# Kernel tuning notes

Hardware: AMD Instinct MI355X
Metric: run time of the kernel (lower is better)

## Reference

```python
import jax, jax.numpy as jnp
import numpy as np

N = 50000        # nodes
E = 800000       # edges (avg degree 16)
HID = 96         # hidden_channels
HEADS = 4        # heads passed to SRGATConv
D = HID // HEADS # per-head dim
R = 38           # num_relations
NEG_SLOPE = 0.2  # LeakyReLU slope for attention logits


def setup_inputs() -> dict:
    key = jax.random.key(0)
    ks = jax.random.split(key, 9)
    x = jax.random.normal(ks[0], (N, HID), jnp.float32)
    edge_index = jax.random.randint(ks[1], (2, E), 0, N, dtype=jnp.int32)
    edge_type = jax.random.randint(ks[2], (E,), 0, R, dtype=jnp.int32)
    s = 1.0 / np.sqrt(HID)
    W = jax.random.normal(ks[3], (HID, HID), jnp.float32) * s          # node projection
    rel_emb = jax.random.normal(ks[4], (R, HID), jnp.float32) * s      # relation embeddings
    att_src = jax.random.normal(ks[5], (HEADS, D), jnp.float32) * 0.1  # attention vectors
    att_dst = jax.random.normal(ks[6], (HEADS, D), jnp.float32) * 0.1
    att_rel = jax.random.normal(ks[7], (HEADS, D), jnp.float32) * 0.1
    bias = jnp.zeros((HID,), jnp.float32)
    return {"x": x, "edge_index": edge_index, "edge_type": edge_type,
            "W": W, "rel_emb": rel_emb, "att_src": att_src,
            "att_dst": att_dst, "att_rel": att_rel, "bias": bias}


def reference(x, edge_index, edge_type, W, rel_emb, att_src, att_dst, att_rel, bias):
    # SRGATConv: relation-aware multi-head graph attention, then GELU wrapper.
    n = x.shape[0]
    src, dst = edge_index[0], edge_index[1]
    h = (x @ W).reshape(n, HEADS, D)                    # [N,H,D]
    r = rel_emb[edge_type].reshape(-1, HEADS, D)        # [E,H,D] gathered relation feats
    h_src = h[src]                                      # [E,H,D] irregular gather
    h_dst = h[dst]
    # attention logits per edge/head
    logits = ((h_src * att_src).sum(-1)
              + (h_dst * att_dst).sum(-1)
              + (r * att_rel).sum(-1))                  # [E,H]
    logits = jax.nn.leaky_relu(logits, NEG_SLOPE)
    # segment softmax over incoming edges of each destination node
    lmax = jax.ops.segment_max(logits, dst, num_segments=n)   # [N,H]
    e = jnp.exp(logits - lmax[dst])
    denom = jax.ops.segment_sum(e, dst, num_segments=n)       # [N,H]
    alpha = e / denom[dst]                                    # [E,H]
    # weighted message scatter
    msg = alpha[:, :, None] * (h_src + r)                     # [E,H,D]
    out = jax.ops.segment_sum(msg, dst, num_segments=n).reshape(n, HID) + bias
    out = jax.nn.gelu(out)
    return out, alpha
```

## Files before the change

kernel.cpp:

```cpp
#include <hip/hip_runtime.h>
#include <hip/hip_fp16.h>
#include <math.h>

#define HIDC 96
#define HEADS 4
#define RMAX 40
#define BINSZ 64
#define BINB 6
#define BINCAP 1344
#define TILE 2048
#define SRCB 18
#define SRCM ((1 << SRCB) - 1)
#define ETB 6
#define NBMAX 1024

typedef unsigned u32x2 __attribute__((ext_vector_type(2)));

__device__ __forceinline__ __half2 u2h2(unsigned u) {
    return *reinterpret_cast<__half2*>(&u);
}
__device__ __forceinline__ unsigned h22u(__half2 h) {
    return *reinterpret_cast<unsigned*>(&h);
}

__global__ __launch_bounds__(192) void gemm96(const float* __restrict__ x,
                                              const float* __restrict__ W,
                                              __half* __restrict__ h16,
                                              int* __restrict__ bincnt,
                                              int4* __restrict__ csrtail,
                                              int n, int nbins) {
    for (int i = blockIdx.x * 192 + threadIdx.x; i < nbins; i += gridDim.x * 192)
        bincnt[i] = 0;
    if (blockIdx.x == 0 && threadIdx.x < 16)
        csrtail[threadIdx.x] = make_int4(0, 0, 0, 0);

    __shared__ float Ws[HIDC * HIDC];
    __shared__ float xs[32 * HIDC];
    for (int i = threadIdx.x; i < HIDC * HIDC / 4; i += 192)
        reinterpret_cast<float4*>(Ws)[i] = reinterpret_cast<const float4*>(W)[i];
    int c4 = threadIdx.x % 24;
    int r0 = (threadIdx.x / 24) * 4;
    const float4* xs4 = reinterpret_cast<const float4*>(xs);
    const float4* Ws4 = reinterpret_cast<const float4*>(Ws);
    uint2* h8 = reinterpret_cast<uint2*>(h16);
    int numTiles = (n + 31) >> 5;
    for (int tile = blockIdx.x; tile < numTiles; tile += gridDim.x) {
        int row0 = tile << 5;
        int rows = min(32, n - row0);
        __syncthreads();
        for (int i = threadIdx.x; i < rows * 24; i += 192)
            reinterpret_cast<float4*>(xs)[i] =
                reinterpret_cast<const float4*>(x + (size_t)row0 * HIDC)[i];
        __syncthreads();
        float4 acc[4];
#pragma unroll
        for (int i = 0; i < 4; ++i) acc[i] = make_float4(0.f, 0.f, 0.f, 0.f);
#pragma unroll 4
        for (int k4 = 0; k4 < 24; ++k4) {
            float4 xv[4], wv[4];
#pragma unroll
            for (int i = 0; i < 4; ++i) xv[i] = xs4[(r0 + i) * 24 + k4];
#pragma unroll
            for (int j = 0; j < 4; ++j) wv[j] = Ws4[(k4 * 4 + j) * 24 + c4];
#pragma unroll
            for (int i = 0; i < 4; ++i) {
                const float xi[4] = {xv[i].x, xv[i].y, xv[i].z, xv[i].w};
#pragma unroll
                for (int j = 0; j < 4; ++j) {
                    acc[i].x = fmaf(xi[j], wv[j].x, acc[i].x);
                    acc[i].y = fmaf(xi[j], wv[j].y, acc[i].y);
                    acc[i].z = fmaf(xi[j], wv[j].z, acc[i].z);
                    acc[i].w = fmaf(xi[j], wv[j].w, acc[i].w);
                }
            }
        }
#pragma unroll
        for (int i = 0; i < 4; ++i)
            if (r0 + i < rows) {
                __half2 lo = __floats2half2_rn(acc[i].x, acc[i].y);
                __half2 hi = __floats2half2_rn(acc[i].z, acc[i].w);
                uint2 pk;
                pk.x = h22u(lo);
                pk.y = h22u(hi);
                h8[(size_t)(row0 + r0 + i) * 24 + c4] = pk;
            }
    }
}

__global__ __launch_bounds__(256) void node_dots(
    const __half* __restrict__ h16,
    const float* __restrict__ att_src, const float* __restrict__ att_dst,
    const float* __restrict__ rel, const float* __restrict__ att_rel,
    float4* __restrict__ ps, float* __restrict__ pdi,
    float4* __restrict__ pr, int n, int R_) {
    if (blockIdx.x == gridDim.x - 1) {
        int t = threadIdx.x;
        if (t < R_) {
            const float4* rp = reinterpret_cast<const float4*>(rel + (size_t)t * HIDC);
            const float4* ar = reinterpret_cast<const float4*>(att_rel);
            float acc[HEADS] = {0, 0, 0, 0};
#pragma unroll
            for (int c = 0; c < 24; ++c) {
                float4 v = rp[c], a = ar[c];
                acc[c / 6] += v.x * a.x + v.y * a.y + v.z * a.z + v.w * a.w;
            }
            pr[t] = make_float4(acc[0], acc[1], acc[2], acc[3]);
        }
        return;
    }
    int i = blockIdx.x * blockDim.x + threadIdx.x;
    if (i >= n) return;
    const uint2* hp = reinterpret_cast<const uint2*>(h16 + (size_t)i * HIDC);
    const float4* as = reinterpret_cast<const float4*>(att_src);
    const float4* ad = reinterpret_cast<const float4*>(att_dst);
    float accs[HEADS] = {0, 0, 0, 0}, accd[HEADS] = {0, 0, 0, 0};
#pragma unroll
    for (int c = 0; c < 24; ++c) {
        uint2 hv = hp[c];
        float2 f0 = __half22float2(u2h2(hv.x));
        float2 f1 = __half22float2(u2h2(hv.y));
        float4 a = as[c], d = ad[c];
        int hh = c / 6;
        accs[hh] += f0.x * a.x + f0.y * a.y + f1.x * a.z + f1.y * a.w;
        accd[hh] += f0.x * d.x + f0.y * d.y + f1.x * d.z + f1.y * d.w;
    }
    ps[i] = make_float4(accs[0], accs[1], accs[2], accs[3]);
    *reinterpret_cast<float4*>(pdi + (size_t)i * 8) =
        make_float4(accd[0], accd[1], accd[2], accd[3]);
}

__device__ __forceinline__ float4 ev4(float4 a, float4 b, float4 c) {
    float l0 = a.x + b.x + c.x, l1 = a.y + b.y + c.y;
    float l2 = a.z + b.z + c.z, l3 = a.w + b.w + c.w;
    l0 = l0 >= 0.f ? l0 : 0.2f * l0;
    l1 = l1 >= 0.f ? l1 : 0.2f * l1;
    l2 = l2 >= 0.f ? l2 : 0.2f * l2;
    l3 = l3 >= 0.f ? l3 : 0.2f * l3;
    return make_float4(__expf(l0), __expf(l1), __expf(l2), __expf(l3));
}

__device__ __forceinline__ float gelu_f(float v) {
    float u = 0.7978845608028654f * (v + 0.044715f * v * v * v);
    u = fminf(fmaxf(u, -15.f), 15.f);
    float t = __expf(2.f * u);
    return 0.5f * v * (1.f + (t - 1.f) / (t + 1.f));
}

__global__ __launch_bounds__(256) void bin_edges(
    const int* __restrict__ src, const int* __restrict__ dst,
    const int* __restrict__ et,
    int* __restrict__ bincnt, int* __restrict__ binwords,
    int E_, int nbins) {
    __shared__ int hist[NBMAX];
    __shared__ int base[NBMAX];
    int e0 = blockIdx.x * TILE;
    for (int i = threadIdx.x; i < nbins; i += 256) hist[i] = 0;
    __syncthreads();
    int mybin[8], myrank[8], myword[8];
#pragma unroll
    for (int u = 0; u < 8; ++u) {
        int e = e0 + u * 256 + threadIdx.x;
        mybin[u] = -1;
        if (e < E_) {
            int d = dst[e];
            int b = d >> BINB;
            myword[u] = src[e] | (et[e] << SRCB) | ((d & (BINSZ - 1)) << (SRCB + ETB));
            mybin[u] = b;
            myrank[u] = atomicAdd(&hist[b], 1);
        }
    }
    __syncthreads();
    for (int i = threadIdx.x; i < nbins; i += 256)
        base[i] = hist[i] > 0 ? atomicAdd(&bincnt[i], hist[i]) : 0;
    __syncthreads();
#pragma unroll
    for (int u = 0; u < 8; ++u) {
        if (mybin[u] >= 0) {
            int pos = base[mybin[u]] + myrank[u];
            if (pos < BINCAP)
                binwords[(size_t)mybin[u] * BINCAP + pos] = myword[u];
        }
    }
}

__global__ __launch_bounds__(256) void bin_sort(
    const int* __restrict__ bincnt, const int* __restrict__ binwords,
    const float4* __restrict__ ps, const float* __restrict__ pdi,
    const float4* __restrict__ prg,
    int4* __restrict__ csr, int* __restrict__ noff, int* __restrict__ ncnt,
    int n, int R_) {
    __shared__ int cnts[BINSZ];
    __shared__ int scanb[BINSZ];
    __shared__ int nbase[BINSZ];
    __shared__ float4 pdl[BINSZ];
    __shared__ float4 prl[RMAX];
    int bin = blockIdx.x;
    int node0 = bin * BINSZ;
    int total = min(bincnt[bin], BINCAP);

    for (int i = threadIdx.x; i < BINSZ; i += 256) {
        cnts[i] = 0;
        int nd = node0 + i;
        pdl[i] = (nd < n) ? *reinterpret_cast<const float4*>(pdi + (size_t)nd * 8)
                          : make_float4(0.f, 0.f, 0.f, 0.f);
    }
    for (int i = threadIdx.x; i < R_; i += 256) prl[i] = prg[i];
    __syncthreads();

    int w[6], rk[6];
#pragma unroll
    for (int u = 0; u < 6; ++u) {
        int k = u * 256 + threadIdx.x;
        rk[u] = -1;
        if (k < total) {
            w[u] = binwords[(size_t)bin * BINCAP + k];
            int dl = (w[u] >> (SRCB + ETB)) & (BINSZ - 1);
            rk[u] = atomicAdd(&cnts[dl], 1);
        }
    }
    __syncthreads();

    if (threadIdx.x < BINSZ) scanb[threadIdx.x] = (cnts[threadIdx.x] + 3) & ~3;
    __syncthreads();
    for (int s = 1; s < BINSZ; s <<= 1) {
        int v = 0;
        if (threadIdx.x < BINSZ && threadIdx.x >= s) v = scanb[threadIdx.x - s];
        __syncthreads();
        if (threadIdx.x < BINSZ) scanb[threadIdx.x] += v;
        __syncthreads();
    }
    if (threadIdx.x < BINSZ) {
        int cnt = cnts[threadIdx.x];
        int cntP = (cnt + 3) & ~3;
        int nb = scanb[threadIdx.x] - cntP;
        nbase[threadIdx.x] = nb;
        int nd = node0 + threadIdx.x;
        if (nd < n) {
            noff[nd] = bin * BINCAP + nb;
            ncnt[nd] = cnt;
        }
        int4 z = make_int4(0, 0, 0, 0);
        for (int i = cnt; i < cntP; ++i)
            csr[(size_t)bin * BINCAP + nb + i] = z;
    }
    {
        int gt = scanb[BINSZ - 1];
        if (threadIdx.x < 12) {
            int p = gt + threadIdx.x;
            if (p < BINCAP)
                csr[(size_t)bin * BINCAP + p] = make_int4(0, 0, 0, 0);
        }
    }
    __syncthreads();

#pragma unroll
    for (int u = 0; u < 6; ++u) {
        if (rk[u] >= 0) {
            int s = w[u] & SRCM;
            int t = (w[u] >> SRCB) & ((1 << ETB) - 1);
            int dl = (w[u] >> (SRCB + ETB)) & (BINSZ - 1);
            float4 v = ev4(ps[s], pdl[dl], prl[t]);
            int4 pk;
            pk.x = s * (HIDC * 2);
            pk.y = t * (HIDC * 2);
            pk.z = (int)h22u(__floats2half2_rn(v.x, v.y));
            pk.w = (int)h22u(__floats2half2_rn(v.z, v.w));
            csr[(size_t)bin * BINCAP + nbase[dl] + rk[u]] = pk;
        }
    }
}

__global__ __launch_bounds__(256) void node_agg(
    const __half* __restrict__ h16, const float* __restrict__ rel,
    const int4* __restrict__ csr, const int* __restrict__ noff,
    const int* __restrict__ ncnt,
    float* __restrict__ pdi, const float* __restrict__ bias,
    float* __restrict__ out, int n, int R_) {
    __shared__ uint2 relh[RMAX * HIDC / 4];
    for (int i = threadIdx.x; i < R_ * 24; i += 256) {
        float4 v = reinterpret_cast<const float4*>(rel)[i];
        uint2 pk;
        pk.x = h22u(__floats2half2_rn(v.x, v.y));
        pk.y = h22u(__floats2half2_rn(v.z, v.w));
        relh[i] = pk;
    }
    __syncthreads();

    int lane = threadIdx.x & 31;
    if (lane >= 24) return;
    const int j = lane;
    const int j4 = 4 * j;
    const int hh = j / 6;
    const unsigned joff = (unsigned)(j << 3);
    const float4 bv = *reinterpret_cast<const float4*>(bias + j4);
    const char* h16c = reinterpret_cast<const char*>(h16);
    const char* relc = reinterpret_cast<const char*>(relh);
    const unsigned esel = (unsigned)(2 * hh) | ((unsigned)(2 * hh + 1) << 8);

    int hw0 = (blockIdx.x * blockDim.x + threadIdx.x) >> 5;
    int nHW = (gridDim.x * blockDim.x) >> 5;

    for (int hw = hw0; hw < n; hw += nHW) {
        int cnt = ncnt[hw];
        const int4* sp = csr + noff[hw];
        float a0 = 0.f, a1 = 0.f, a2 = 0.f, a3 = 0.f;
        float dsum = 0.f;

        if (cnt > 0) {
            int cntP = (cnt + 3) & ~3;
            int4 pc[4];
#pragma unroll
            for (int u = 0; u < 4; ++u) pc[u] = sp[u];
            sp += 4;

            for (int k = 0; k < cntP; k += 4, sp += 4) {
                uint2 hv[4], rv[4];
#pragma unroll
                for (int u = 0; u < 4; ++u)
                    hv[u] = *reinterpret_cast<const uint2*>(
                        h16c + (unsigned)pc[u].x + joff);
#pragma unroll
                for (int u = 0; u < 4; ++u)
                    rv[u] = *reinterpret_cast<const uint2*>(
                        relc + (unsigned)pc[u].y + joff);
                int4 pn[4];
#pragma unroll
                for (int u = 0; u < 4; ++u) pn[u] = sp[u];
#pragma unroll
                for (int u = 0; u < 4; ++u) {
                    unsigned e32 = __builtin_amdgcn_perm(
                        (unsigned)pc[u].w, (unsigned)pc[u].z, esel);
                    dsum += __half2float(__low2half(u2h2(e32)));
                    unsigned s01 = h22u(__hadd2(u2h2(hv[u].x), u2h2(rv[u].x)));
                    unsigned s23 = h22u(__hadd2(u2h2(hv[u].y), u2h2(rv[u].y)));
                    asm("v_fma_mix_f32 %0, %1, %2, %0 op_sel:[0,0,0] op_sel_hi:[1,1,0]"
                        : "+v"(a0) : "v"(s01), "v"(e32));
                    asm("v_fma_mix_f32 %0, %1, %2, %0 op_sel:[1,0,0] op_sel_hi:[1,1,0]"
                        : "+v"(a1) : "v"(s01), "v"(e32));
                    asm("v_fma_mix_f32 %0, %1, %2, %0 op_sel:[0,0,0] op_sel_hi:[1,1,0]"
                        : "+v"(a2) : "v"(s23), "v"(e32));
                    asm("v_fma_mix_f32 %0, %1, %2, %0 op_sel:[1,0,0] op_sel_hi:[1,1,0]"
                        : "+v"(a3) : "v"(s23), "v"(e32));
                }
#pragma unroll
                for (int u = 0; u < 4; ++u) pc[u] = pn[u];
            }
        }
        float inv = dsum > 0.f ? 1.f / dsum : 0.f;
        if ((j % 6) == 0) pdi[(size_t)hw * 8 + 4 + hh] = inv;
        float4 o;
        o.x = gelu_f(a0 * inv + bv.x);
        o.y = gelu_f(a1 * inv + bv.y);
        o.z = gelu_f(a2 * inv + bv.z);
        o.w = gelu_f(a3 * inv + bv.w);
        *reinterpret_cast<float4*>(out + (size_t)hw * HIDC + j4) = o;
    }
}

__global__ void alpha_edge(const int* __restrict__ src, const int* __restrict__ dst,
                           const int* __restrict__ et,
                           const float4* __restrict__ ps, const float* __restrict__ pdi,
                           const float4* __restrict__ pr,
                           float4* __restrict__ alpha, int E_) {
    int e = blockIdx.x * blockDim.x + threadIdx.x;
    if (e >= E_) return;
    int d = dst[e];
    const float4* rec = reinterpret_cast<const float4*>(pdi + (size_t)d * 8);
    float4 b = rec[0];
    float4 iv = rec[1];
    float4 v = ev4(ps[src[e]], b, pr[et[e]]);
    alpha[e] = make_float4(v.x * iv.x, v.y * iv.y, v.z * iv.z, v.w * iv.w);
}

extern "C" void kernel_launch(void* const* d_in, const int* in_sizes, int n_in,
                              void* d_out, int out_size, void* d_ws, size_t ws_size,
                              hipStream_t stream) {
    const float* x       = (const float*)d_in[0];
    const int*   eidx    = (const int*)d_in[1];
    const int*   etype   = (const int*)d_in[2];
    const float* W       = (const float*)d_in[3];
    const float* rel     = (const float*)d_in[4];
    const float* att_src = (const float*)d_in[5];
    const float* att_dst = (const float*)d_in[6];
    const float* att_rel = (const float*)d_in[7];
    const float* bias    = (const float*)d_in[8];

    int N_ = in_sizes[0] / HIDC;
    int E_ = in_sizes[1] / 2;
    int R_ = in_sizes[4] / HIDC;
    const int* src  = eidx;
    const int* dstp = eidx + E_;
    int nbins = (N_ + BINSZ - 1) / BINSZ;

    char* ws = (char*)d_ws;
    __half* h16      = (__half*)ws; ws += (size_t)N_ * HIDC * 2;
    float4* ps       = (float4*)ws; ws += (size_t)N_ * 16;
    float*  pdi      = (float*)ws;  ws += (size_t)N_ * 32;
    float4* pr       = (float4*)ws; ws += 1024;
    int*    bincnt   = (int*)ws;    ws += (size_t)((nbins + 3) & ~3) * 4;
    int*    noff     = (int*)ws;    ws += (size_t)((N_ + 3) & ~3) * 4;
    int*    ncnt     = (int*)ws;    ws += (size_t)((N_ + 3) & ~3) * 4;
    int*    binwords = (int*)ws;    ws += (size_t)nbins * BINCAP * 4;
    int4*   csr      = (int4*)ws;   ws += (size_t)nbins * BINCAP * 16 + 256;

    float*  outv  = (float*)d_out;
    float4* alpha = (float4*)(outv + (size_t)N_ * HIDC);

    gemm96<<<(N_ + 31) / 32, 192, 0, stream>>>(
        x, W, h16, bincnt, csr + (size_t)nbins * BINCAP, N_, nbins);

    node_dots<<<(N_ + 255) / 256 + 1, 256, 0, stream>>>(
        h16, att_src, att_dst, rel, att_rel, ps, pdi, pr, N_, R_);

    bin_edges<<<(E_ + TILE - 1) / TILE, 256, 0, stream>>>(
        src, dstp, etype, bincnt, binwords, E_, nbins);

    bin_sort<<<nbins, 256, 0, stream>>>(
        bincnt, binwords, ps, pdi, pr, csr, noff, ncnt, N_, R_);

    node_agg<<<(N_ + 15) / 16, 256, 0, stream>>>(
        h16, rel, csr, noff, ncnt, pdi, bias, outv, N_, R_);

    alpha_edge<<<(E_ + 255) / 256, 256, 0, stream>>>(
        src, dstp, etype, ps, pdi, pr, alpha, E_);
}
```

Baseline: 203.6 us.

## Fuse alpha output into node aggregation by packing edge ids into CSR entries

Removes the separate alpha_edge kernel. Each CSR record now carries the original edge id in the spare high bits of its source and relation offsets, and node_agg writes alpha for each incoming edge from the stored fp16 exp values times the per-head inverse denominator. This drops the second gather of src/dst/type and the pdi/ps lookups across all edges. In exchange, binwords doubles in size, alpha becomes a scattered write, it uses fp16-rounded exp values, and the bit packing assumes the edge count fits in 8+19 bits.

Result: faster. 192.6 us (-5.4%).

```diff
diff --git a/kernel.cpp b/kernel.cpp
--- a/kernel.cpp
+++ b/kernel.cpp
@@ -149,7 +149,7 @@
 __global__ __launch_bounds__(256) void bin_edges(
     const int* __restrict__ src, const int* __restrict__ dst,
     const int* __restrict__ et,
-    int* __restrict__ bincnt, int* __restrict__ binwords,
+    int* __restrict__ bincnt, int2* __restrict__ binwords,
     int E_, int nbins) {
     __shared__ int hist[NBMAX];
     __shared__ int base[NBMAX];
@@ -178,13 +178,14 @@
         if (mybin[u] >= 0) {
             int pos = base[mybin[u]] + myrank[u];
             if (pos < BINCAP)
-                binwords[(size_t)mybin[u] * BINCAP + pos] = myword[u];
+                binwords[(size_t)mybin[u] * BINCAP + pos] =
+                    make_int2(myword[u], e0 + u * 256 + threadIdx.x);
         }
     }
 }
 
 __global__ __launch_bounds__(256) void bin_sort(
-    const int* __restrict__ bincnt, const int* __restrict__ binwords,
+    const int* __restrict__ bincnt, const int2* __restrict__ binwords,
     const float4* __restrict__ ps, const float* __restrict__ pdi,
     const float4* __restrict__ prg,
     int4* __restrict__ csr, int* __restrict__ noff, int* __restrict__ ncnt,
@@ -207,14 +208,15 @@
     for (int i = threadIdx.x; i < R_; i += 256) prl[i] = prg[i];
     __syncthreads();
 
-    int w[6], rk[6];
+    int2 w[6];
+    int rk[6];
 #pragma unroll
     for (int u = 0; u < 6; ++u) {
         int k = u * 256 + threadIdx.x;
         rk[u] = -1;
         if (k < total) {
             w[u] = binwords[(size_t)bin * BINCAP + k];
-            int dl = (w[u] >> (SRCB + ETB)) & (BINSZ - 1);
+            int dl = (w[u].x >> (SRCB + ETB)) & (BINSZ - 1);
             rk[u] = atomicAdd(&cnts[dl], 1);
         }
     }
@@ -256,13 +258,14 @@
 #pragma unroll
     for (int u = 0; u < 6; ++u) {
         if (rk[u] >= 0) {
-            int s = w[u] & SRCM;
-            int t = (w[u] >> SRCB) & ((1 << ETB) - 1);
-            int dl = (w[u] >> (SRCB + ETB)) & (BINSZ - 1);
+            int s = w[u].x & SRCM;
+            int t = (w[u].x >> SRCB) & ((1 << ETB) - 1);
+            int dl = (w[u].x >> (SRCB + ETB)) & (BINSZ - 1);
+            unsigned e = (unsigned)w[u].y;
             float4 v = ev4(ps[s], pdl[dl], prl[t]);
             int4 pk;
-            pk.x = s * (HIDC * 2);
-            pk.y = t * (HIDC * 2);
+            pk.x = (int)((unsigned)(s * (HIDC * 2)) | ((e & 0xFFu) << 24));
+            pk.y = (int)((unsigned)(t * (HIDC * 2)) | ((e >> 8) << 13));
             pk.z = (int)h22u(__floats2half2_rn(v.x, v.y));
             pk.w = (int)h22u(__floats2half2_rn(v.z, v.w));
             csr[(size_t)bin * BINCAP + nbase[dl] + rk[u]] = pk;
@@ -274,8 +277,8 @@
     const __half* __restrict__ h16, const float* __restrict__ rel,
     const int4* __restrict__ csr, const int* __restrict__ noff,
     const int* __restrict__ ncnt,
-    float* __restrict__ pdi, const float* __restrict__ bias,
-    float* __restrict__ out, int n, int R_) {
+    const float* __restrict__ bias,
+    float* __restrict__ out, float4* __restrict__ alpha, int n, int R_) {
     __shared__ uint2 relh[RMAX * HIDC / 4];
     for (int i = threadIdx.x; i < R_ * 24; i += 256) {
         float4 v = reinterpret_cast<const float4*>(rel)[i];
@@ -302,7 +305,8 @@
 
     for (int hw = hw0; hw < n; hw += nHW) {
         int cnt = ncnt[hw];
-        const int4* sp = csr + noff[hw];
+        const int4* sp0 = csr + noff[hw];
+        const int4* sp = sp0;
         float a0 = 0.f, a1 = 0.f, a2 = 0.f, a3 = 0.f;
         float dsum = 0.f;
 
@@ -318,11 +322,11 @@
 #pragma unroll
                 for (int u = 0; u < 4; ++u)
                     hv[u] = *reinterpret_cast<const uint2*>(
-                        h16c + (unsigned)pc[u].x + joff);
+                        h16c + ((unsigned)pc[u].x & 0x00FFFFFFu) + joff);
 #pragma unroll
                 for (int u = 0; u < 4; ++u)
                     rv[u] = *reinterpret_cast<const uint2*>(
-                        relc + (unsigned)pc[u].y + joff);
+                        relc + ((unsigned)pc[u].y & 0x1FFFu) + joff);
                 int4 pn[4];
 #pragma unroll
                 for (int u = 0; u < 4; ++u) pn[u] = sp[u];
@@ -347,29 +351,28 @@
             }
         }
         float inv = dsum > 0.f ? 1.f / dsum : 0.f;
-        if ((j % 6) == 0) pdi[(size_t)hw * 8 + 4 + hh] = inv;
         float4 o;
         o.x = gelu_f(a0 * inv + bv.x);
         o.y = gelu_f(a1 * inv + bv.y);
         o.z = gelu_f(a2 * inv + bv.z);
         o.w = gelu_f(a3 * inv + bv.w);
         *reinterpret_cast<float4*>(out + (size_t)hw * HIDC + j4) = o;
-    }
-}
-
-__global__ void alpha_edge(const int* __restrict__ src, const int* __restrict__ dst,
-                           const int* __restrict__ et,
-                           const float4* __restrict__ ps, const float* __restrict__ pdi,
-                           const float4* __restrict__ pr,
-                           float4* __restrict__ alpha, int E_) {
-    int e = blockIdx.x * blockDim.x + threadIdx.x;
-    if (e >= E_) return;
-    int d = dst[e];
-    const float4* rec = reinterpret_cast<const float4*>(pdi + (size_t)d * 8);
-    float4 b = rec[0];
-    float4 iv = rec[1];
-    float4 v = ev4(ps[src[e]], b, pr[et[e]]);
-    alpha[e] = make_float4(v.x * iv.x, v.y * iv.y, v.z * iv.z, v.w * iv.w);
+
+        if (cnt > 0) {
+            float iv0 = __shfl(inv, 0, 32);
+            float iv1 = __shfl(inv, 6, 32);
+            float iv2 = __shfl(inv, 12, 32);
+            float iv3 = __shfl(inv, 18, 32);
+            for (int k = j; k < cnt; k += 24) {
+                int4 pk = sp0[k];
+                unsigned e_id = ((unsigned)pk.x >> 24) | (((unsigned)pk.y >> 13) << 8);
+                float2 f01 = __half22float2(u2h2((unsigned)pk.z));
+                float2 f23 = __half22float2(u2h2((unsigned)pk.w));
+                alpha[e_id] = make_float4(f01.x * iv0, f01.y * iv1,
+                                          f23.x * iv2, f23.y * iv3);
+            }
+        }
+    }
 }
 
 extern "C" void kernel_launch(void* const* d_in, const int* in_sizes, int n_in,
@@ -400,7 +403,7 @@
     int*    bincnt   = (int*)ws;    ws += (size_t)((nbins + 3) & ~3) * 4;
     int*    noff     = (int*)ws;    ws += (size_t)((N_ + 3) & ~3) * 4;
     int*    ncnt     = (int*)ws;    ws += (size_t)((N_ + 3) & ~3) * 4;
-    int*    binwords = (int*)ws;    ws += (size_t)nbins * BINCAP * 4;
+    int2*   binwords = (int2*)ws;   ws += (size_t)nbins * BINCAP * 8;
     int4*   csr      = (int4*)ws;   ws += (size_t)nbins * BINCAP * 16 + 256;
 
     float*  outv  = (float*)d_out;
@@ -419,8 +422,5 @@
         bincnt, binwords, ps, pdi, pr, csr, noff, ncnt, N_, R_);
 
     node_agg<<<(N_ + 15) / 16, 256, 0, stream>>>(
-        h16, rel, csr, noff, ncnt, pdi, bias, outv, N_, R_);
-
-    alpha_edge<<<(E_ + 255) / 256, 256, 0, stream>>>(
-        src, dstp, etype, ps, pdi, pr, alpha, E_);
-}
+        h16, rel, csr, noff, ncnt, bias, outv, alpha, N_, R_);
+}
```
